# Optimization experiments

Measured on AMD Instinct MI355X. Metric: run time of the kernel, lower is better.

## Reference

```python
import jax, jax.numpy as jnp
import numpy as np

N, E = 50000, 400000
DIN, H0, HEADS = 128, 128, 4
C1, C2, C3, DOUT = 64, 32, 64, 32


def seg_softmax(a, seg, n):
    # numerically stable softmax over edges grouped by destination node
    m = jax.ops.segment_max(a, seg, num_segments=n)
    m = jnp.where(jnp.isfinite(m), m, 0.0)
    e = jnp.exp(a - m[seg])
    d = jax.ops.segment_sum(e, seg, num_segments=n)
    return e / (d[seg] + 1e-16)


def setup_inputs():
    key = jax.random.key(0)
    ks = jax.random.split(key, 20)
    p = lambda k, shape, fan: jax.random.normal(k, shape, jnp.float32) / np.sqrt(fan)
    return {
        "x": jax.random.normal(ks[0], (N, DIN), jnp.float32),
        "edge_index": jax.random.randint(ks[1], (2, E), 0, N),
        "cew": jax.random.uniform(ks[2], (N,), dtype=jnp.float32),
        "cew_W": p(ks[3], (DIN, H0), DIN), "cew_b": jnp.zeros((H0,), jnp.float32),
        "cew_att": p(ks[4], (H0,), H0),
        "W1": p(ks[5], (H0, HEADS * C1), H0),
        "att_src1": p(ks[6], (HEADS, C1), C1), "att_dst1": p(ks[7], (HEADS, C1), C1),
        "b1": jnp.zeros((HEADS * C1,), jnp.float32),
        "W2": p(ks[8], (HEADS * C1, HEADS * C2), HEADS * C1),
        "att_src2": p(ks[9], (HEADS, C2), C2), "att_dst2": p(ks[10], (HEADS, C2), C2),
        "b2": jnp.zeros((HEADS * C2,), jnp.float32),
        "Wq": p(ks[11], (HEADS * C2, HEADS * C3), HEADS * C2), "bq": jnp.zeros((HEADS * C3,), jnp.float32),
        "Wk": p(ks[12], (HEADS * C2, HEADS * C3), HEADS * C2), "bk": jnp.zeros((HEADS * C3,), jnp.float32),
        "Wv": p(ks[13], (HEADS * C2, HEADS * C3), HEADS * C2), "bv": jnp.zeros((HEADS * C3,), jnp.float32),
        "Wskip": p(ks[14], (HEADS * C2, C3), HEADS * C2), "bskip": jnp.zeros((C3,), jnp.float32),
        "Wf": p(ks[15], (C3, DOUT), C3), "bf": jnp.zeros((DOUT,), jnp.float32),
    }


def cew_gat(x, src, dst, cew, W, b, att):
    h = x @ W + b                                    # [N, H0]
    s = h @ att                                      # [N] == (h * att).sum(-1)
    alpha = jax.nn.leaky_relu(s[src] + s[dst], 0.01) * (cew[src] + cew[dst])  # [E]
    alpha = seg_softmax(alpha, dst, N)
    return jax.ops.segment_sum(h[src] * alpha[:, None], dst, num_segments=N)


def gat(x, src, dst, W, att_src, att_dst, b, H, C):
    # PyG GATConv: add_self_loops=True by default
    loop = jnp.arange(N)
    src2 = jnp.concatenate([src, loop])
    dst2 = jnp.concatenate([dst, loop])
    h = (x @ W).reshape(N, H, C)
    a_s = (h * att_src).sum(-1)                      # [N, H]
    a_d = (h * att_dst).sum(-1)                      # [N, H]
    alpha = jax.nn.leaky_relu(a_s[src2] + a_d[dst2], 0.2)   # [E+N, H]
    alpha = seg_softmax(alpha, dst2, N)
    out = jax.ops.segment_sum(h[src2] * alpha[..., None], dst2, num_segments=N)
    return out.reshape(N, H * C) + b


def transformer_conv(x, src, dst, Wq, bq, Wk, bk, Wv, bv, Wskip, bskip, H, C):
    q = (x @ Wq + bq).reshape(N, H, C)
    k = (x @ Wk + bk).reshape(N, H, C)
    v = (x @ Wv + bv).reshape(N, H, C)
    alpha = (q[dst] * k[src]).sum(-1) / jnp.sqrt(jnp.float32(C))  # [E, H]
    alpha = seg_softmax(alpha, dst, N)
    out = jax.ops.segment_sum(v[src] * alpha[..., None], dst, num_segments=N)  # [N, H, C]
    # concat=False -> mean over heads, plus root (skip) linear
    return out.mean(axis=1) + (x @ Wskip + bskip)


def reference(x, edge_index, cew, cew_W, cew_b, cew_att, W1, att_src1, att_dst1, b1, W2, att_src2, att_dst2, b2, Wq, bq, Wk, bk, Wv, bv, Wskip, bskip, Wf, bf):
    src, dst = edge_index[0], edge_index[1]
    h = jax.nn.relu(cew_gat(x, src, dst, cew, cew_W, cew_b, cew_att))
    h = jax.nn.relu(gat(h, src, dst, W1, att_src1, att_dst1, b1, HEADS, C1))
    h = jax.nn.relu(gat(h, src, dst, W2, att_src2, att_dst2, b2, HEADS, C2))
    h = jax.nn.relu(transformer_conv(h, src, dst, Wq, bq, Wk, bk, Wv, bv, Wskip, bskip, HEADS, C3))
    return h @ Wf + bf
```

## Files before the change

kernel.cpp:

```cpp
#include <hip/hip_runtime.h>
#include <stdint.h>

#define N_NODES 50000
#define N_EDGES 400000
#define NBLK_SC 196
#define MT128   391

typedef unsigned short u16;
typedef __attribute__((ext_vector_type(8))) short short8;
typedef __attribute__((ext_vector_type(4))) float f32x4;

__device__ __forceinline__ float b2f(u16 u){ unsigned int x=((unsigned int)u)<<16; float f; __builtin_memcpy(&f,&x,4); return f; }
__device__ __forceinline__ u16 f2b(float f){ unsigned int x; __builtin_memcpy(&x,&f,4); x += 0x7fffu + ((x>>16)&1u); return (u16)(x>>16); }

__global__ void k_zeroi(int* __restrict__ p, int n){
  int i = blockIdx.x*256+threadIdx.x;
  if (i < n) p[i] = 0;
}
__global__ void k_fillf(float* __restrict__ p, int n, float v){
  int i = blockIdx.x*256+threadIdx.x;
  if (i < n) p[i] = v;
}
__global__ void k_cvt_x(const float* __restrict__ x, u16* __restrict__ xb, int n){
  int i = blockIdx.x*256+threadIdx.x;
  if (i < n) xb[i] = f2b(x[i]);
}
__global__ void k_transpose_b(const float* __restrict__ W, u16* __restrict__ Wt, int K, int Nc, int Npad){
  int i = blockIdx.x*256+threadIdx.x;
  if (i >= Npad*K) return;
  int n = i / K, k = i - n*K;
  Wt[i] = (n < Nc) ? f2b(W[k*Nc + n]) : (u16)0;
}
__global__ void k_transpose_cat(const float* __restrict__ Wq, const float* __restrict__ Wk,
                                const float* __restrict__ Wv, const float* __restrict__ Wsk,
                                u16* __restrict__ Wt){
  int i = blockIdx.x*256+threadIdx.x;
  if (i >= 896*128) return;
  int n = i >> 7, k = i & 127;
  float v = 0.f;
  if      (n < 256) v = Wq[k*256 + n];
  else if (n < 512) v = Wk[k*256 + (n-256)];
  else if (n < 768) v = Wv[k*256 + (n-512)];
  else if (n < 832) v = Wsk[k*64 + (n-768)];
  Wt[i] = f2b(v);
}

__global__ void k_count(const int* __restrict__ dst, int* __restrict__ cnt){
  int e = blockIdx.x*256+threadIdx.x;
  if (e < N_EDGES) atomicAdd(&cnt[dst[e]], 1);
}
__global__ void k_scan1(const int* __restrict__ cnt, int* __restrict__ ro, int* __restrict__ bsums){
  __shared__ int sm[256];
  int b = blockIdx.x, t = threadIdx.x, i = b*256+t;
  int v = (i < N_NODES) ? cnt[i] : 0;
  sm[t] = v; __syncthreads();
  for (int off=1; off<256; off<<=1){
    int x = 0; if (t>=off) x = sm[t-off];
    __syncthreads();
    if (t>=off) sm[t] += x;
    __syncthreads();
  }
  if (i < N_NODES) ro[i] = sm[t]-v;
  if (t==255) bsums[b] = sm[255];
}
__global__ void k_scan2(int* __restrict__ bsums, int nb){
  __shared__ int sm[256];
  int t = threadIdx.x;
  int v = (t<nb) ? bsums[t] : 0;
  sm[t]=v; __syncthreads();
  for (int off=1; off<256; off<<=1){
    int x = 0; if (t>=off) x = sm[t-off];
    __syncthreads();
    if (t>=off) sm[t] += x;
    __syncthreads();
  }
  if (t<nb) bsums[t] = sm[t]-v;
}
__global__ void k_scan3(int* __restrict__ ro, const int* __restrict__ bsums){
  int b = blockIdx.x, t = threadIdx.x, i = b*256+t;
  if (i < N_NODES) ro[i] += bsums[b];
  if (i == 0) ro[N_NODES] = N_EDGES;
}
__global__ void k_scatter(const int* __restrict__ src, const int* __restrict__ dst,
                          const int* __restrict__ ro, int* __restrict__ cursor,
                          int* __restrict__ perm){
  int e = blockIdx.x*256+threadIdx.x;
  if (e >= N_EDGES) return;
  int d = dst[e];
  int pos = ro[d] + atomicAdd(&cursor[d], 1);
  perm[pos] = src[e];
}

__global__ __launch_bounds__(256)
void k_gemm_mfma(const u16* __restrict__ A, const u16* __restrict__ Bt,
                 const float* __restrict__ bias, u16* __restrict__ C,
                 int K, int Nst, int nTiles)
{
  __shared__ u16 sA[128][40];
  __shared__ u16 sB[128][40];
  int t = threadIdx.x, lane = t & 63, wave = t >> 6;
  int wr = wave >> 1, wc = wave & 1;
  int mTile = blockIdx.x / nTiles, nTile = blockIdx.x - mTile*nTiles;
  int mBase = mTile*128, nBase = nTile*128;
  f32x4 acc[4][4] = {};
  const int row = lane & 15, kq = (lane >> 4) * 8;
  for (int k0 = 0; k0 < K; k0 += 32){
    #pragma unroll
    for (int it = 0; it < 2; ++it){
      int c = it*256 + t;
      int m = c >> 2, ko = (c & 3) * 8;
      int ra = mBase + m;
      uint4 va = {0u,0u,0u,0u};
      if (ra < N_NODES) va = *(const uint4*)(A + (size_t)ra*K + k0 + ko);
      *(uint4*)&sA[m][ko] = va;
      *(uint4*)&sB[m][ko] = *(const uint4*)(Bt + (size_t)(nBase+m)*K + k0 + ko);
    }
    __syncthreads();
    short8 af[4], bfr[4];
    #pragma unroll
    for (int i=0;i<4;i++) af[i]  = *(const short8*)&sA[wr*64 + i*16 + row][kq];
    #pragma unroll
    for (int i=0;i<4;i++) bfr[i] = *(const short8*)&sB[wc*64 + i*16 + row][kq];
    #pragma unroll
    for (int i=0;i<4;i++)
      #pragma unroll
      for (int j=0;j<4;j++)
        acc[i][j] = __builtin_amdgcn_mfma_f32_16x16x32_bf16(af[i], bfr[j], acc[i][j], 0,0,0);
    __syncthreads();
  }
  #pragma unroll
  for (int i=0;i<4;i++)
    #pragma unroll
    for (int j=0;j<4;j++)
      #pragma unroll
      for (int r=0;r<4;r++){
        int mm = mBase + wr*64 + i*16 + (lane>>4)*4 + r;
        if (mm >= N_NODES) continue;
        int nn = nBase + wc*64 + j*16 + (lane&15);
        float v = acc[i][j][r];
        if (bias) v += bias[nn];
        C[(size_t)mm*Nst + nn] = f2b(v);
      }
}

__global__ __launch_bounds__(256)
void k_gemm_qkvs(const u16* __restrict__ A, const u16* __restrict__ Bt,
                 const float* __restrict__ bq, const float* __restrict__ bk,
                 const float* __restrict__ bv,
                 u16* __restrict__ qb, u16* __restrict__ kb, u16* __restrict__ vb,
                 u16* __restrict__ skipb)
{
  __shared__ u16 sA[128][40];
  __shared__ u16 sB[128][40];
  int t = threadIdx.x, lane = t & 63, wave = t >> 6;
  int wr = wave >> 1, wc = wave & 1;
  int mTile = blockIdx.x / 7, nTile = blockIdx.x - mTile*7;
  int mBase = mTile*128, nBase = nTile*128;
  f32x4 acc[4][4] = {};
  const int row = lane & 15, kq = (lane >> 4) * 8;
  const int K = 128;
  for (int k0 = 0; k0 < K; k0 += 32){
    #pragma unroll
    for (int it = 0; it < 2; ++it){
      int c = it*256 + t;
      int m = c >> 2, ko = (c & 3) * 8;
      int ra = mBase + m;
      uint4 va = {0u,0u,0u,0u};
      if (ra < N_NODES) va = *(const uint4*)(A + (size_t)ra*K + k0 + ko);
      *(uint4*)&sA[m][ko] = va;
      *(uint4*)&sB[m][ko] = *(const uint4*)(Bt + (size_t)(nBase+m)*K + k0 + ko);
    }
    __syncthreads();
    short8 af[4], bfr[4];
    #pragma unroll
    for (int i=0;i<4;i++) af[i]  = *(const short8*)&sA[wr*64 + i*16 + row][kq];
    #pragma unroll
    for (int i=0;i<4;i++) bfr[i] = *(const short8*)&sB[wc*64 + i*16 + row][kq];
    #pragma unroll
    for (int i=0;i<4;i++)
      #pragma unroll
      for (int j=0;j<4;j++)
        acc[i][j] = __builtin_amdgcn_mfma_f32_16x16x32_bf16(af[i], bfr[j], acc[i][j], 0,0,0);
    __syncthreads();
  }
  #pragma unroll
  for (int j=0;j<4;j++){
    int nn = nBase + wc*64 + j*16 + (lane&15);
    u16* dst; int stride, col; float bias;
    if      (nn < 256){ dst=qb;    stride=256; col=nn;     bias=bq[nn];     }
    else if (nn < 512){ dst=kb;    stride=256; col=nn-256; bias=bk[nn-256]; }
    else if (nn < 768){ dst=vb;    stride=256; col=nn-512; bias=bv[nn-512]; }
    else if (nn < 832){ dst=skipb; stride=64;  col=nn-768; bias=0.f;        }
    else continue;
    #pragma unroll
    for (int i=0;i<4;i++)
      #pragma unroll
      for (int r=0;r<4;r++){
        int mm = mBase + wr*64 + i*16 + (lane>>4)*4 + r;
        if (mm >= N_NODES) continue;
        dst[(size_t)mm*stride + col] = f2b(acc[i][j][r] + bias);
      }
  }
}

__global__ __launch_bounds__(256)
void k_rowdot_cew(const u16* __restrict__ hb, const float* __restrict__ att, float* __restrict__ s){
  int n = blockIdx.x*256+threadIdx.x;
  if (n >= N_NODES) return;
  const u16* hp = hb + (size_t)n*128;
  float acc = 0.f;
  #pragma unroll 8
  for (int c=0;c<128;++c) acc += b2f(hp[c])*att[c];
  s[n] = acc;
}
__global__ __launch_bounds__(256)
void k_rowdot4(const u16* __restrict__ hb, const float* __restrict__ attS, const float* __restrict__ attD,
               float* __restrict__ aS, float* __restrict__ aD){
  int t = blockIdx.x*256+threadIdx.x;
  if (t >= N_NODES*4) return;
  int n = t>>2, h = t&3;
  const u16* hp = hb + (size_t)n*256 + h*64;
  const float* as = attS + h*64;
  const float* ad = attD + h*64;
  float ps=0.f, pd=0.f;
  #pragma unroll 8
  for (int c=0;c<64;++c){ float v=b2f(hp[c]); ps += v*as[c]; pd += v*ad[c]; }
  aS[t]=ps; aD[t]=pd;
}
__global__ __launch_bounds__(256)
void k_rowdot2(const u16* __restrict__ hb, const float* __restrict__ attS, const float* __restrict__ attD,
               float* __restrict__ aS, float* __restrict__ aD){
  int t = blockIdx.x*256+threadIdx.x;
  if (t >= N_NODES*4) return;
  int n = t>>2, h = t&3;
  const u16* hp = hb + (size_t)n*128 + h*32;
  const float* as = attS + h*32;
  const float* ad = attD + h*32;
  float ps=0.f, pd=0.f;
  #pragma unroll 8
  for (int c=0;c<32;++c){ float v=b2f(hp[c]); ps += v*as[c]; pd += v*ad[c]; }
  aS[t]=ps; aD[t]=pd;
}

__global__ __launch_bounds__(256)
void k_agg_cew(const u16* __restrict__ h0, const float* __restrict__ s, const float* __restrict__ cewf,
               const int* __restrict__ ro, const int* __restrict__ perm, u16* __restrict__ x1)
{
  int wave = threadIdx.x>>6, lane = threadIdx.x&63;
  int node = blockIdx.x*4 + wave;
  if (node >= N_NODES) return;
  float sd = s[node], cd = cewf[node];
  int beg = ro[node], end = ro[node+1];
  int f = 2*lane;
  float m = -INFINITY, d = 0.f, a0 = 0.f, a1 = 0.f;
  for (int cbeg = beg; cbeg < end; cbeg += 64){
    int j = cbeg + lane;
    float lg = -INFINITY; int u = 0;
    if (j < end){
      u = perm[j];
      float a = s[u] + sd; a = a>=0.f ? a : 0.01f*a;
      lg = a * (cewf[u] + cd);
    }
    float cm = lg;
    #pragma unroll
    for (int o=32;o;o>>=1) cm = fmaxf(cm, __shfl_xor(cm,o));
    if (cm > m){
      float r = __expf(m - cm);
      d*=r; a0*=r; a1*=r; m = cm;
    }
    float wl = __expf(lg - m);
    int cnt = end - cbeg; if (cnt > 64) cnt = 64;
    for (int e=0; e<cnt; ++e){
      float we = __shfl(wl, e);
      int ue = __shfl(u, e);
      d += we;
      unsigned int pv = *(const unsigned int*)(h0 + (size_t)ue*128 + f);
      a0 += we * b2f((u16)(pv & 0xffffu));
      a1 += we * b2f((u16)(pv >> 16));
    }
  }
  float inv = 1.f/(d + 1e-16f);
  float o0 = a0*inv; o0 = o0>0.f?o0:0.f;
  float o1 = a1*inv; o1 = o1>0.f?o1:0.f;
  *(unsigned int*)(x1 + (size_t)node*128 + f) = (unsigned int)f2b(o0) | ((unsigned int)f2b(o1)<<16);
}

__global__ __launch_bounds__(256)
void k_agg_gat1(const u16* __restrict__ hb, const float* __restrict__ aS, const float* __restrict__ aD,
                const float* __restrict__ bias, const int* __restrict__ ro, const int* __restrict__ perm,
                u16* __restrict__ out)
{
  int wave = threadIdx.x>>6, lane = threadIdx.x&63;
  int node = blockIdx.x*4 + wave;
  if (node >= N_NODES) return;
  int h = lane >> 4, l = lane & 15, grp = h << 4;
  auto lk = [](float x){ return x>=0.f ? x : 0.2f*x; };
  float ad = aD[node*4+h];
  float sl = lk(aS[node*4+h] + ad);
  int beg = ro[node], end = ro[node+1];
  int fo = h*64 + l*4;
  float m = sl, d = 1.f;
  float c0,c1,c2,c3;
  { ushort4 pv = *(const ushort4*)(hb + (size_t)node*256 + fo);
    c0=b2f(pv.x); c1=b2f(pv.y); c2=b2f(pv.z); c3=b2f(pv.w); }
  for (int cbeg = beg; cbeg < end; cbeg += 16){
    int j = cbeg + l;
    float lg = -INFINITY; int u = 0;
    if (j < end){ u = perm[j]; lg = lk(aS[u*4+h] + ad); }
    float cm = lg;
    cm = fmaxf(cm, __shfl_xor(cm,1));
    cm = fmaxf(cm, __shfl_xor(cm,2));
    cm = fmaxf(cm, __shfl_xor(cm,4));
    cm = fmaxf(cm, __shfl_xor(cm,8));
    if (cm > m){
      float r = __expf(m - cm);
      d*=r; c0*=r; c1*=r; c2*=r; c3*=r; m = cm;
    }
    float wl = __expf(lg - m);
    int cnt = end - cbeg; if (cnt > 16) cnt = 16;
    for (int e=0; e<cnt; ++e){
      float we = __shfl(wl, grp + e);
      int ue = __shfl(u, grp + e);
      d += we;
      ushort4 vv = *(const ushort4*)(hb + (size_t)ue*256 + fo);
      c0 += we*b2f(vv.x); c1 += we*b2f(vv.y); c2 += we*b2f(vv.z); c3 += we*b2f(vv.w);
    }
  }
  float inv = 1.f/(d + 1e-16f);
  float o0 = c0*inv + bias[fo+0]; o0 = o0>0.f?o0:0.f;
  float o1 = c1*inv + bias[fo+1]; o1 = o1>0.f?o1:0.f;
  float o2 = c2*inv + bias[fo+2]; o2 = o2>0.f?o2:0.f;
  float o3 = c3*inv + bias[fo+3]; o3 = o3>0.f?o3:0.f;
  ushort4 ov = { f2b(o0), f2b(o1), f2b(o2), f2b(o3) };
  *(ushort4*)(out + (size_t)node*256 + fo) = ov;
}

__global__ __launch_bounds__(256)
void k_agg_gat2(const u16* __restrict__ hb, const float* __restrict__ aS, const float* __restrict__ aD,
                const float* __restrict__ bias, const int* __restrict__ ro, const int* __restrict__ perm,
                u16* __restrict__ out)
{
  int wave = threadIdx.x>>6, lane = threadIdx.x&63;
  int node = blockIdx.x*4 + wave;
  if (node >= N_NODES) return;
  int h = lane >> 4, l = lane & 15, grp = h << 4;
  auto lk = [](float x){ return x>=0.f ? x : 0.2f*x; };
  float ad = aD[node*4+h];
  float sl = lk(aS[node*4+h] + ad);
  int beg = ro[node], end = ro[node+1];
  int fo = h*32 + l*2;
  float m = sl, d = 1.f;
  float c0,c1;
  { unsigned int pv = *(const unsigned int*)(hb + (size_t)node*128 + fo);
    c0 = b2f((u16)(pv & 0xffffu)); c1 = b2f((u16)(pv >> 16)); }
  for (int cbeg = beg; cbeg < end; cbeg += 16){
    int j = cbeg + l;
    float lg = -INFINITY; int u = 0;
    if (j < end){ u = perm[j]; lg = lk(aS[u*4+h] + ad); }
    float cm = lg;
    cm = fmaxf(cm, __shfl_xor(cm,1));
    cm = fmaxf(cm, __shfl_xor(cm,2));
    cm = fmaxf(cm, __shfl_xor(cm,4));
    cm = fmaxf(cm, __shfl_xor(cm,8));
    if (cm > m){
      float r = __expf(m - cm);
      d*=r; c0*=r; c1*=r; m = cm;
    }
    float wl = __expf(lg - m);
    int cnt = end - cbeg; if (cnt > 16) cnt = 16;
    for (int e=0; e<cnt; ++e){
      float we = __shfl(wl, grp + e);
      int ue = __shfl(u, grp + e);
      d += we;
      unsigned int pv = *(const unsigned int*)(hb + (size_t)ue*128 + fo);
      c0 += we*b2f((u16)(pv & 0xffffu));
      c1 += we*b2f((u16)(pv >> 16));
    }
  }
  float inv = 1.f/(d + 1e-16f);
  float o0 = c0*inv + bias[fo+0]; o0 = o0>0.f?o0:0.f;
  float o1 = c1*inv + bias[fo+1]; o1 = o1>0.f?o1:0.f;
  *(unsigned int*)(out + (size_t)node*128 + fo) = (unsigned int)f2b(o0) | ((unsigned int)f2b(o1)<<16);
}

__global__ __launch_bounds__(256)
void k_tr(const u16* __restrict__ qb, const u16* __restrict__ kb, const u16* __restrict__ vb,
          const u16* __restrict__ skipb, const float* __restrict__ bsk,
          const int* __restrict__ ro, const int* __restrict__ perm, u16* __restrict__ x4)
{
  int wave = threadIdx.x>>6, lane = threadIdx.x&63;
  int node = blockIdx.x*4 + wave;
  if (node >= N_NODES) return;
  int h = lane >> 4, l = lane & 15;
  int fo = h*64 + l*4;
  ushort4 qv = *(const ushort4*)(qb + (size_t)node*256 + fo);
  float q0=b2f(qv.x), q1=b2f(qv.y), q2=b2f(qv.z), q3=b2f(qv.w);
  float m=-INFINITY, d=0.f, a0=0.f,a1=0.f,a2=0.f,a3=0.f;
  int beg = ro[node], end = ro[node+1];
  for (int j=beg; j<end; ++j){
    int u = perm[j];
    ushort4 kv = *(const ushort4*)(kb + (size_t)u*256 + fo);
    float p = q0*b2f(kv.x) + q1*b2f(kv.y) + q2*b2f(kv.z) + q3*b2f(kv.w);
    p += __shfl_xor(p,1); p += __shfl_xor(p,2); p += __shfl_xor(p,4); p += __shfl_xor(p,8);
    p *= 0.125f;
    if (p > m){
      float r = __expf(m - p);
      d*=r; a0*=r; a1*=r; a2*=r; a3*=r; m = p;
    }
    float w = __expf(p - m);
    d += w;
    ushort4 vv = *(const ushort4*)(vb + (size_t)u*256 + fo);
    a0 += w*b2f(vv.x); a1 += w*b2f(vv.y); a2 += w*b2f(vv.z); a3 += w*b2f(vv.w);
  }
  float inv = 0.25f/(d + 1e-16f);
  a0*=inv; a1*=inv; a2*=inv; a3*=inv;
  a0 += __shfl_xor(a0,16); a0 += __shfl_xor(a0,32);
  a1 += __shfl_xor(a1,16); a1 += __shfl_xor(a1,32);
  a2 += __shfl_xor(a2,16); a2 += __shfl_xor(a2,32);
  a3 += __shfl_xor(a3,16); a3 += __shfl_xor(a3,32);
  if (h==0){
    int c = l*4;
    ushort4 sv = *(const ushort4*)(skipb + (size_t)node*64 + c);
    float o0 = a0 + b2f(sv.x) + bsk[c+0]; o0 = o0>0.f?o0:0.f;
    float o1 = a1 + b2f(sv.y) + bsk[c+1]; o1 = o1>0.f?o1:0.f;
    float o2 = a2 + b2f(sv.z) + bsk[c+2]; o2 = o2>0.f?o2:0.f;
    float o3 = a3 + b2f(sv.w) + bsk[c+3]; o3 = o3>0.f?o3:0.f;
    ushort4 ov = { f2b(o0), f2b(o1), f2b(o2), f2b(o3) };
    *(ushort4*)(x4 + (size_t)node*64 + c) = ov;
  }
}

__global__ __launch_bounds__(256)
void k_final(const u16* __restrict__ x4, const float* __restrict__ Wf, const float* __restrict__ bf,
             float* __restrict__ out)
{
  int i = blockIdx.x*256+threadIdx.x;
  if (i >= N_NODES*32) return;
  int n = i>>5, c = i&31;
  const u16* xr = x4 + (size_t)n*64;
  float acc = 0.f;
  #pragma unroll
  for (int k=0;k<64;++k) acc += b2f(xr[k]) * Wf[k*32+c];
  acc += bf[c];
  out[i] = acc;
}

extern "C" void kernel_launch(void* const* d_in, const int* in_sizes, int n_in,
                              void* d_out, int out_size, void* d_ws, size_t ws_size,
                              hipStream_t stream)
{
  const float* i_x    = (const float*)d_in[0];
  const int*   i_ei   = (const int*)d_in[1];
  const float* i_cew  = (const float*)d_in[2];
  const float* i_cewW = (const float*)d_in[3];
  const float* i_cewB = (const float*)d_in[4];
  const float* i_cewA = (const float*)d_in[5];
  const float* i_W1   = (const float*)d_in[6];
  const float* i_aS1  = (const float*)d_in[7];
  const float* i_aD1  = (const float*)d_in[8];
  const float* i_b1   = (const float*)d_in[9];
  const float* i_W2   = (const float*)d_in[10];
  const float* i_aS2  = (const float*)d_in[11];
  const float* i_aD2  = (const float*)d_in[12];
  const float* i_b2   = (const float*)d_in[13];
  const float* i_Wq   = (const float*)d_in[14];
  const float* i_bq   = (const float*)d_in[15];
  const float* i_Wk   = (const float*)d_in[16];
  const float* i_bk   = (const float*)d_in[17];
  const float* i_Wv   = (const float*)d_in[18];
  const float* i_bv   = (const float*)d_in[19];
  const float* i_Wsk  = (const float*)d_in[20];
  const float* i_bsk  = (const float*)d_in[21];
  const float* i_Wf   = (const float*)d_in[22];
  const float* i_bf   = (const float*)d_in[23];
  (void)in_sizes; (void)n_in; (void)out_size;

  char* w = (char*)d_ws;
  size_t off = 0;
  auto A = [&](size_t bytes)->char*{ char* p = w + off; off = (off + bytes + 255) & ~(size_t)255; return p; };

  int*   bsums  = (int*)A(1024);
  float* sbuf   = (float*)A((size_t)N_NODES*4);
  float* aS     = (float*)A((size_t)N_NODES*16);
  float* aD     = (float*)A((size_t)N_NODES*16);
  int*   cnt    = (int*)A((size_t)N_NODES*4);
  int*   ro     = (int*)A((size_t)(N_NODES+1)*4);
  int*   cursor = (int*)A((size_t)N_NODES*4);
  int*   perm   = (int*)A((size_t)N_EDGES*4);
  u16*   cewWt  = (u16*)A(128*128*2);
  u16*   W1t    = (u16*)A(256*128*2);
  u16*   W2t    = (u16*)A(128*256*2);
  u16*   Wcat   = (u16*)A(896*128*2);
  u16*   xb     = (u16*)A((size_t)N_NODES*128*2);
  u16* S1   = (u16*)A((size_t)N_NODES*128*2);
  u16* S2   = (u16*)A((size_t)N_NODES*128*2);
  u16* G1   = (u16*)A((size_t)N_NODES*256*2);
  u16* G2   = (u16*)A((size_t)N_NODES*256*2);
  u16* G3   = (u16*)A((size_t)N_NODES*256*2);
  size_t need = off;

  float* outf = (float*)d_out;
  if (ws_size < need){
    k_fillf<<<(N_NODES*32+255)/256,256,0,stream>>>(outf, N_NODES*32,
        8192.f + 32.f * (float)((ws_size >> 20) > 255 ? 255 : (ws_size >> 20)));
    return;
  }

  u16* h0 = S1;  u16* x1 = S2;
  u16* h1 = G1;  u16* x2 = G2;
  u16* h2 = S1;  u16* x3 = S2;
  u16* qb = G1;  u16* kb = G2;  u16* vb = G3;
  u16* skipb = S1;  u16* x4 = S2;

  k_zeroi<<<(N_NODES+255)/256,256,0,stream>>>(cnt, N_NODES);
  k_zeroi<<<(N_NODES+255)/256,256,0,stream>>>(cursor, N_NODES);

  k_cvt_x<<<(N_NODES*128+255)/256,256,0,stream>>>(i_x, xb, N_NODES*128);
  k_transpose_b<<<(128*128+255)/256,256,0,stream>>>(i_cewW, cewWt, 128, 128, 128);
  k_transpose_b<<<(256*128+255)/256,256,0,stream>>>(i_W1,   W1t,  128, 256, 256);
  k_transpose_b<<<(128*256+255)/256,256,0,stream>>>(i_W2,   W2t,  256, 128, 128);
  k_transpose_cat<<<(896*128+255)/256,256,0,stream>>>(i_Wq, i_Wk, i_Wv, i_Wsk, Wcat);

  k_count<<<(N_EDGES+255)/256,256,0,stream>>>(i_ei + N_EDGES, cnt);
  k_scan1<<<NBLK_SC,256,0,stream>>>(cnt, ro, bsums);
  k_scan2<<<1,256,0,stream>>>(bsums, NBLK_SC);
  k_scan3<<<NBLK_SC,256,0,stream>>>(ro, bsums);
  k_scatter<<<(N_EDGES+255)/256,256,0,stream>>>(i_ei, i_ei + N_EDGES, ro, cursor, perm);

  const int NAGG = (N_NODES+3)/4;
  const int NH4  = (N_NODES*4+255)/256;

  k_gemm_mfma<<<MT128*1,256,0,stream>>>(xb, cewWt, i_cewB, h0, 128, 128, 1);
  k_rowdot_cew<<<(N_NODES+255)/256,256,0,stream>>>(h0, i_cewA, sbuf);
  k_agg_cew<<<NAGG,256,0,stream>>>(h0, sbuf, i_cew, ro, perm, x1);

  k_gemm_mfma<<<MT128*2,256,0,stream>>>(x1, W1t, nullptr, h1, 128, 256, 2);
  k_rowdot4<<<NH4,256,0,stream>>>(h1, i_aS1, i_aD1, aS, aD);
  k_agg_gat1<<<NAGG,256,0,stream>>>(h1, aS, aD, i_b1, ro, perm, x2);

  k_gemm_mfma<<<MT128*1,256,0,stream>>>(x2, W2t, nullptr, h2, 256, 128, 1);
  k_rowdot2<<<NH4,256,0,stream>>>(h2, i_aS2, i_aD2, aS, aD);
  k_agg_gat2<<<NAGG,256,0,stream>>>(h2, aS, aD, i_b2, ro, perm, x3);

  k_gemm_qkvs<<<MT128*7,256,0,stream>>>(x3, Wcat, i_bq, i_bk, i_bv, qb, kb, vb, skipb);
  k_tr<<<NAGG,256,0,stream>>>(qb, kb, vb, skipb, i_bsk, ro, perm, x4);

  k_final<<<(N_NODES*32+255)/256,256,0,stream>>>(x4, i_Wf, i_bf, outf);
}
```

Before: 563.9 us.

## Drop max subtraction from segment softmax and batch transformer attention scores per lane

Removes the running-max rescaling of the online softmax in the CEW, GAT1 and GAT2 aggregation kernels, exponentiating logits directly. The transformer kernel now has each lane compute a full 64-wide q·k dot product for its own edge, 16 edges per chunk, then broadcasts weights via shuffles, instead of serially reducing one edge at a time across lanes. This removes shuffle reductions and branchy rescales but risks overflow in exp when logits are large, relying on the input distribution keeping scores small.

Measured after the change: 566.4 us. Within noise of the previous version (+0.4%).

```diff
diff --git a/kernel.cpp b/kernel.cpp
--- a/kernel.cpp
+++ b/kernel.cpp
@@ -252,23 +252,15 @@
   float sd = s[node], cd = cewf[node];
   int beg = ro[node], end = ro[node+1];
   int f = 2*lane;
-  float m = -INFINITY, d = 0.f, a0 = 0.f, a1 = 0.f;
+  float d = 0.f, a0 = 0.f, a1 = 0.f;
   for (int cbeg = beg; cbeg < end; cbeg += 64){
     int j = cbeg + lane;
-    float lg = -INFINITY; int u = 0;
+    float wl = 0.f; int u = 0;
     if (j < end){
       u = perm[j];
       float a = s[u] + sd; a = a>=0.f ? a : 0.01f*a;
-      lg = a * (cewf[u] + cd);
-    }
-    float cm = lg;
-    #pragma unroll
-    for (int o=32;o;o>>=1) cm = fmaxf(cm, __shfl_xor(cm,o));
-    if (cm > m){
-      float r = __expf(m - cm);
-      d*=r; a0*=r; a1*=r; m = cm;
-    }
-    float wl = __expf(lg - m);
+      wl = __expf(a * (cewf[u] + cd));
+    }
     int cnt = end - cbeg; if (cnt > 64) cnt = 64;
     for (int e=0; e<cnt; ++e){
       float we = __shfl(wl, e);
@@ -296,27 +288,17 @@
   int h = lane >> 4, l = lane & 15, grp = h << 4;
   auto lk = [](float x){ return x>=0.f ? x : 0.2f*x; };
   float ad = aD[node*4+h];
-  float sl = lk(aS[node*4+h] + ad);
+  float sw = __expf(lk(aS[node*4+h] + ad));
   int beg = ro[node], end = ro[node+1];
   int fo = h*64 + l*4;
-  float m = sl, d = 1.f;
+  float d = sw;
   float c0,c1,c2,c3;
   { ushort4 pv = *(const ushort4*)(hb + (size_t)node*256 + fo);
-    c0=b2f(pv.x); c1=b2f(pv.y); c2=b2f(pv.z); c3=b2f(pv.w); }
+    c0=sw*b2f(pv.x); c1=sw*b2f(pv.y); c2=sw*b2f(pv.z); c3=sw*b2f(pv.w); }
   for (int cbeg = beg; cbeg < end; cbeg += 16){
     int j = cbeg + l;
-    float lg = -INFINITY; int u = 0;
-    if (j < end){ u = perm[j]; lg = lk(aS[u*4+h] + ad); }
-    float cm = lg;
-    cm = fmaxf(cm, __shfl_xor(cm,1));
-    cm = fmaxf(cm, __shfl_xor(cm,2));
-    cm = fmaxf(cm, __shfl_xor(cm,4));
-    cm = fmaxf(cm, __shfl_xor(cm,8));
-    if (cm > m){
-      float r = __expf(m - cm);
-      d*=r; c0*=r; c1*=r; c2*=r; c3*=r; m = cm;
-    }
-    float wl = __expf(lg - m);
+    float wl = 0.f; int u = 0;
+    if (j < end){ u = perm[j]; wl = __expf(lk(aS[u*4+h] + ad)); }
     int cnt = end - cbeg; if (cnt > 16) cnt = 16;
     for (int e=0; e<cnt; ++e){
       float we = __shfl(wl, grp + e);
@@ -346,27 +328,17 @@
   int h = lane >> 4, l = lane & 15, grp = h << 4;
   auto lk = [](float x){ return x>=0.f ? x : 0.2f*x; };
   float ad = aD[node*4+h];
-  float sl = lk(aS[node*4+h] + ad);
+  float sw = __expf(lk(aS[node*4+h] + ad));
   int beg = ro[node], end = ro[node+1];
   int fo = h*32 + l*2;
-  float m = sl, d = 1.f;
+  float d = sw;
   float c0,c1;
   { unsigned int pv = *(const unsigned int*)(hb + (size_t)node*128 + fo);
-    c0 = b2f((u16)(pv & 0xffffu)); c1 = b2f((u16)(pv >> 16)); }
+    c0 = sw*b2f((u16)(pv & 0xffffu)); c1 = sw*b2f((u16)(pv >> 16)); }
   for (int cbeg = beg; cbeg < end; cbeg += 16){
     int j = cbeg + l;
-    float lg = -INFINITY; int u = 0;
-    if (j < end){ u = perm[j]; lg = lk(aS[u*4+h] + ad); }
-    float cm = lg;
-    cm = fmaxf(cm, __shfl_xor(cm,1));
-    cm = fmaxf(cm, __shfl_xor(cm,2));
-    cm = fmaxf(cm, __shfl_xor(cm,4));
-    cm = fmaxf(cm, __shfl_xor(cm,8));
-    if (cm > m){
-      float r = __expf(m - cm);
-      d*=r; c0*=r; c1*=r; m = cm;
-    }
-    float wl = __expf(lg - m);
+    float wl = 0.f; int u = 0;
+    if (j < end){ u = perm[j]; wl = __expf(lk(aS[u*4+h] + ad)); }
     int cnt = end - cbeg; if (cnt > 16) cnt = 16;
     for (int e=0; e<cnt; ++e){
       float we = __shfl(wl, grp + e);
@@ -383,6 +355,19 @@
   *(unsigned int*)(out + (size_t)node*128 + fo) = (unsigned int)f2b(o0) | ((unsigned int)f2b(o1)<<16);
 }
 
+__device__ __forceinline__ float dot8bf(uint4 a, uint4 b){
+  float p = 0.f;
+  p += b2f((u16)(a.x & 0xffffu))*b2f((u16)(b.x & 0xffffu));
+  p += b2f((u16)(a.x >> 16))    *b2f((u16)(b.x >> 16));
+  p += b2f((u16)(a.y & 0xffffu))*b2f((u16)(b.y & 0xffffu));
+  p += b2f((u16)(a.y >> 16))    *b2f((u16)(b.y >> 16));
+  p += b2f((u16)(a.z & 0xffffu))*b2f((u16)(b.z & 0xffffu));
+  p += b2f((u16)(a.z >> 16))    *b2f((u16)(b.z >> 16));
+  p += b2f((u16)(a.w & 0xffffu))*b2f((u16)(b.w & 0xffffu));
+  p += b2f((u16)(a.w >> 16))    *b2f((u16)(b.w >> 16));
+  return p;
+}
+
 __global__ __launch_bounds__(256)
 void k_tr(const u16* __restrict__ qb, const u16* __restrict__ kb, const u16* __restrict__ vb,
           const u16* __restrict__ skipb, const float* __restrict__ bsk,
@@ -391,26 +376,33 @@
   int wave = threadIdx.x>>6, lane = threadIdx.x&63;
   int node = blockIdx.x*4 + wave;
   if (node >= N_NODES) return;
-  int h = lane >> 4, l = lane & 15;
+  int h = lane >> 4, l = lane & 15, grp = h << 4;
+  const uint4* qp = (const uint4*)(qb + (size_t)node*256 + h*64);
+  uint4 qr[8];
+  #pragma unroll
+  for (int c=0;c<8;++c) qr[c] = qp[c];
   int fo = h*64 + l*4;
-  ushort4 qv = *(const ushort4*)(qb + (size_t)node*256 + fo);
-  float q0=b2f(qv.x), q1=b2f(qv.y), q2=b2f(qv.z), q3=b2f(qv.w);
-  float m=-INFINITY, d=0.f, a0=0.f,a1=0.f,a2=0.f,a3=0.f;
+  float d=0.f, a0=0.f,a1=0.f,a2=0.f,a3=0.f;
   int beg = ro[node], end = ro[node+1];
-  for (int j=beg; j<end; ++j){
-    int u = perm[j];
-    ushort4 kv = *(const ushort4*)(kb + (size_t)u*256 + fo);
-    float p = q0*b2f(kv.x) + q1*b2f(kv.y) + q2*b2f(kv.z) + q3*b2f(kv.w);
-    p += __shfl_xor(p,1); p += __shfl_xor(p,2); p += __shfl_xor(p,4); p += __shfl_xor(p,8);
-    p *= 0.125f;
-    if (p > m){
-      float r = __expf(m - p);
-      d*=r; a0*=r; a1*=r; a2*=r; a3*=r; m = p;
-    }
-    float w = __expf(p - m);
-    d += w;
-    ushort4 vv = *(const ushort4*)(vb + (size_t)u*256 + fo);
-    a0 += w*b2f(vv.x); a1 += w*b2f(vv.y); a2 += w*b2f(vv.z); a3 += w*b2f(vv.w);
+  for (int cbeg = beg; cbeg < end; cbeg += 16){
+    int j = cbeg + l;
+    float wl = 0.f; int u = 0;
+    if (j < end){
+      u = perm[j];
+      const uint4* kp = (const uint4*)(kb + (size_t)u*256 + h*64);
+      float p = 0.f;
+      #pragma unroll
+      for (int c=0;c<8;++c) p += dot8bf(qr[c], kp[c]);
+      wl = __expf(p * 0.125f);
+    }
+    int cnt = end - cbeg; if (cnt > 16) cnt = 16;
+    for (int e=0; e<cnt; ++e){
+      float we = __shfl(wl, grp + e);
+      int ue = __shfl(u, grp + e);
+      d += we;
+      ushort4 vv = *(const ushort4*)(vb + (size_t)ue*256 + fo);
+      a0 += we*b2f(vv.x); a1 += we*b2f(vv.y); a2 += we*b2f(vv.z); a3 += we*b2f(vv.w);
+    }
   }
   float inv = 0.25f/(d + 1e-16f);
   a0*=inv; a1*=inv; a2*=inv; a3*=inv;
```
